# Kernel tuning notes

Hardware: AMD Instinct MI355X
Metric: run time of the kernel (lower is better)

## Reference

```python
import jax, jax.numpy as jnp
from jax import lax
import numpy as np

B, T, I, H = 8192, 365, 3, 34


def setup_inputs() -> dict:
    key = jax.random.key(0)
    ks = jax.random.split(key, 7)
    s_in = 1.0 / np.sqrt(I)
    s_h = 1.0 / np.sqrt(H)
    return {
        "x": jax.random.normal(ks[0], (B, T, I), dtype=jnp.float32),
        "fc0_w": jax.random.uniform(ks[1], (H, I), jnp.float32, -s_in, s_in),
        "fc0_b": jax.random.uniform(ks[2], (H,), jnp.float32, -s_in, s_in),
        "w_ih": jax.random.uniform(ks[3], (4 * H, H), jnp.float32, -s_h, s_h),
        "w_hh": jax.random.uniform(ks[4], (4 * H, H), jnp.float32, -s_h, s_h),
        "b_ih": jax.random.uniform(ks[5], (4 * H,), jnp.float32, -s_h, s_h),
        "b_hh": jax.random.uniform(ks[6], (4 * H,), jnp.float32, -s_h, s_h),
    }


def reference(x, fc0_w, fc0_b, w_ih, w_hh, b_ih, b_hh):
    # fc0: [B,T,I] -> [B,T,H]
    l1 = jnp.einsum("bti,hi->bth", x, fc0_w) + fc0_b
    # Precompute input-side gate projections for all timesteps: [B,T,4H]
    gx = jnp.einsum("bth,gh->btg", l1, w_ih) + b_ih + b_hh
    gx_t = jnp.swapaxes(gx, 0, 1)  # [T,B,4H]

    h0 = jnp.zeros((x.shape[0], fc0_w.shape[0]), dtype=x.dtype)
    c0 = h0

    def step(carry, g_t):
        h, c = carry
        gates = g_t + h @ w_hh.T  # [B,4H]
        i, f, g, o = jnp.split(gates, 4, axis=-1)  # torch gate order: i,f,g,o
        i = jax.nn.sigmoid(i)
        f = jax.nn.sigmoid(f)
        g = jnp.tanh(g)
        o = jax.nn.sigmoid(o)
        c_new = f * c + i * g
        h_new = o * jnp.tanh(c_new)
        return (h_new, c_new), h_new

    (_, _), hs = lax.scan(step, (h0, c0), gx_t)  # hs: [T,B,H]
    return jnp.swapaxes(hs, 0, 1)  # [B,T,H]
```

## Files before the change

kernel.cpp:

```cpp
#include <hip/hip_runtime.h>

namespace {

constexpr int Bn = 8192;
constexpr int Tn = 365;
constexpr int Hn = 34;
constexpr int GB = 16;
constexpr int KP = 72;

constexpr float L2E = 1.44269504088896340736f;

typedef __attribute__((ext_vector_type(8))) _Float16 f16x8;
typedef __attribute__((ext_vector_type(4))) float f32x4;

__device__ __forceinline__ float fexp2(float v) { return __builtin_amdgcn_exp2f(v); }
__device__ __forceinline__ float frcp(float v)  { return __builtin_amdgcn_rcpf(v); }

__device__ __forceinline__ void block_sync_lds() {
    __builtin_amdgcn_sched_barrier(0);
    asm volatile("s_waitcnt lgkmcnt(0)" ::: "memory");
    __builtin_amdgcn_s_barrier();
    __builtin_amdgcn_sched_barrier(0);
}


__global__ __launch_bounds__(256) void lstm_kernel(
    const float* __restrict__ x,
    const float* __restrict__ fc0_w,
    const float* __restrict__ fc0_b,
    const float* __restrict__ w_ih,
    const float* __restrict__ w_hh,
    const float* __restrict__ b_ih,
    const float* __restrict__ b_hh,
    float* __restrict__ out)
{
    __shared__ __align__(16) _Float16 a_lds[2][GB][KP];

    const int tid  = threadIdx.x;
    const int lane = tid & 63;
    const int wv   = tid >> 6;
    const int b    = lane & 15;
    const int kg   = lane >> 4;

    const int nc   = (wv < 2) ? 9 : 8;
    const int base = (wv < 2) ? 9 * wv : 18 + 8 * (wv - 2);

    f16x8 Wt[3][2];
    #pragma unroll
    for (int tau = 0; tau < 3; ++tau) {
        const int rhat = 16 * tau + b;
        const int jl = rhat >> 2, g = rhat & 3;
        const int r = (jl < nc) ? g * Hn + (base + jl) : -1;
        const float s = (g == 2) ? (2.f * L2E) : (-L2E);
        float swc[3] = {0.f, 0.f, 0.f};
        float bia = 0.f;
        if (r >= 0) {
            float ab = 0.f;
            for (int m = 0; m < Hn; ++m) {
                const float wi = w_ih[r * Hn + m];
                swc[0] += wi * fc0_w[m * 3 + 0];
                swc[1] += wi * fc0_w[m * 3 + 1];
                swc[2] += wi * fc0_w[m * 3 + 2];
                ab     += wi * fc0_b[m];
            }
            swc[0] *= s; swc[1] *= s; swc[2] *= s;
            bia = s * (ab + b_ih[r] + b_hh[r]);
        }
        #pragma unroll
        for (int ks = 0; ks < 2; ++ks) {
            f16x8 f;
            #pragma unroll
            for (int e = 0; e < 8; ++e) {
                const int k = ks * 32 + kg * 8 + e;
                float val = 0.f;
                if (r >= 0) {
                    if (k < 34)       val = s * w_hh[r * Hn + k];
                    else if (k < 37)  val = swc[k - 34];
                    else if (k < 40)  val = swc[k - 37];
                    else if (k == 40) val = bia;
                    else if (k == 41) val = bia - (float)(_Float16)bia;
                }
                f[e] = (_Float16)val;
            }
            Wt[tau][ks] = f;
        }
    }

    const bool has2 = (8 + kg < nc);
    float c0 = 0.f, c1 = 0.f, c2 = 0.f;
    float h0 = 0.f, h1 = 0.f, h2 = 0.f;

    const bool xact = (lane < 12);
    const int bx = 4 * wv + lane / 3;
    const int ix = lane - 3 * (lane / 3);

    for (int i = tid; i < 2 * GB * KP; i += 256) ((_Float16*)a_lds)[i] = (_Float16)0.f;
    block_sync_lds();

    const long long bg = (long long)blockIdx.x * GB;
    const float* xblk = x + bg * (long long)(Tn * 3);
    float* oblk = out + bg * (long long)(Tn * Hn);
    const long long TH = (long long)Tn * Hn;

    if (tid < 32) {
        a_lds[tid >> 4][tid & 15][40] = (_Float16)1.f;
        a_lds[tid >> 4][tid & 15][41] = (_Float16)1.f;
    }
    if (xact) {
        const float xr = xblk[bx * (Tn * 3) + ix];
        const _Float16 xh = (_Float16)xr;
        a_lds[0][bx][34 + ix] = xh;
        a_lds[0][bx][37 + ix] = (_Float16)(xr - (float)xh);
    }
    block_sync_lds();

    float xr_hold = 0.f;
    if (xact && 1 < Tn)
        xr_hold = xblk[bx * (Tn * 3) + 3 + ix];

    float* pr = oblk + (long long)b * TH + base;

    for (int t = 0; t < Tn; ++t) {
        const int cur = t & 1, nxt = cur ^ 1;

        f16x8 av[2];
        #pragma unroll
        for (int ks = 0; ks < 2; ++ks)
            av[ks] = *(const f16x8*)(&a_lds[cur][b][ks * 32 + kg * 8]);

        if (xact) {
            const _Float16 xh = (_Float16)xr_hold;
            a_lds[nxt][bx][34 + ix] = xh;
            a_lds[nxt][bx][37 + ix] = (_Float16)(xr_hold - (float)xh);
        }

        if (t) {
            pr[kg]     = h0;
            pr[4 + kg] = h1;
            if (has2) pr[8 + kg] = h2;
            pr += Hn;
        }

        float xr_next = 0.f;
        if (xact && t + 2 < Tn)
            xr_next = xblk[bx * (Tn * 3) + (t + 2) * 3 + ix];

        f32x4 acc[3];
        #pragma unroll
        for (int tau = 0; tau < 3; ++tau) {
            acc[tau] = f32x4{0.f, 0.f, 0.f, 0.f};
            #pragma unroll
            for (int ks = 0; ks < 2; ++ks)
                acc[tau] = __builtin_amdgcn_mfma_f32_16x16x32_f16(Wt[tau][ks], av[ks], acc[tau], 0, 0, 0);
        }

        {
            const float gi = frcp(1.f + fexp2(acc[0][0]));
            const float gf = frcp(1.f + fexp2(acc[0][1]));
            const float gg = fmaf(-2.f, frcp(1.f + fexp2(acc[0][2])), 1.f);
            const float go = frcp(1.f + fexp2(acc[0][3]));
            c0 = gf * c0 + gi * gg;
            h0 = go * fmaf(-2.f, frcp(1.f + fexp2(c0 * (2.f * L2E))), 1.f);
            a_lds[nxt][b][base + kg] = (_Float16)h0;
        }
        {
            const float gi = frcp(1.f + fexp2(acc[1][0]));
            const float gf = frcp(1.f + fexp2(acc[1][1]));
            const float gg = fmaf(-2.f, frcp(1.f + fexp2(acc[1][2])), 1.f);
            const float go = frcp(1.f + fexp2(acc[1][3]));
            c1 = gf * c1 + gi * gg;
            h1 = go * fmaf(-2.f, frcp(1.f + fexp2(c1 * (2.f * L2E))), 1.f);
            a_lds[nxt][b][base + 4 + kg] = (_Float16)h1;
        }
        if (has2) {
            const float gi = frcp(1.f + fexp2(acc[2][0]));
            const float gf = frcp(1.f + fexp2(acc[2][1]));
            const float gg = fmaf(-2.f, frcp(1.f + fexp2(acc[2][2])), 1.f);
            const float go = frcp(1.f + fexp2(acc[2][3]));
            c2 = gf * c2 + gi * gg;
            h2 = go * fmaf(-2.f, frcp(1.f + fexp2(c2 * (2.f * L2E))), 1.f);
            a_lds[nxt][b][base + 8 + kg] = (_Float16)h2;
        }

        xr_hold = xr_next;

        block_sync_lds();
    }

    {
        pr[kg]     = h0;
        pr[4 + kg] = h1;
        if (has2) pr[8 + kg] = h2;
    }
}

}

extern "C" void kernel_launch(void* const* d_in, const int* in_sizes, int n_in,
                              void* d_out, int out_size, void* d_ws, size_t ws_size,
                              hipStream_t stream) {
    const float* x     = (const float*)d_in[0];
    const float* fc0_w = (const float*)d_in[1];
    const float* fc0_b = (const float*)d_in[2];
    const float* w_ih  = (const float*)d_in[3];
    const float* w_hh  = (const float*)d_in[4];
    const float* b_ih  = (const float*)d_in[5];
    const float* b_hh  = (const float*)d_in[6];
    float* out = (float*)d_out;

    lstm_kernel<<<Bn / GB, 256, 0, stream>>>(x, fc0_w, fc0_b, w_ih, w_hh, b_ih, b_hh, out);
}
```

Before: 351.9 us.

## Repartition LSTM cells across 8 waves with 32-batch blocks

Doubles the batch tile per block to 32 and the block size to 512 threads (8 waves). Each wave now owns 4 hidden cells and one gate-weight tile, which it reuses for two batch halves. Wave 7 also handles the last 2 cells. This replaces the old split of 4 waves holding 3 weight tiles each, aiming for fewer wasted MFMA rows and more independent MFMAs per wave. The cost is a heavier load on wave 7 and a block-wide barrier over 8 waves at every timestep.

```diff
diff --git a/kernel.cpp b/kernel.cpp
--- a/kernel.cpp
+++ b/kernel.cpp
@@ -5,7 +5,8 @@
 constexpr int Bn = 8192;
 constexpr int Tn = 365;
 constexpr int Hn = 34;
-constexpr int GB = 16;
+constexpr int GB = 32;
+constexpr int NT = 512;
 constexpr int KP = 72;
 
 constexpr float L2E = 1.44269504088896340736f;
@@ -24,7 +25,7 @@
 }
 
 
-__global__ __launch_bounds__(256) void lstm_kernel(
+__global__ __launch_bounds__(NT) void lstm_kernel(
     const float* __restrict__ x,
     const float* __restrict__ fc0_w,
     const float* __restrict__ fc0_b,
@@ -42,19 +43,19 @@
     const int b    = lane & 15;
     const int kg   = lane >> 4;
 
-    const int nc   = (wv < 2) ? 9 : 8;
-    const int base = (wv < 2) ? 9 * wv : 18 + 8 * (wv - 2);
-
-    f16x8 Wt[3][2];
+    f16x8 Wt[2], Wt2[2];
     #pragma unroll
-    for (int tau = 0; tau < 3; ++tau) {
-        const int rhat = 16 * tau + b;
-        const int jl = rhat >> 2, g = rhat & 3;
-        const int r = (jl < nc) ? g * Hn + (base + jl) : -1;
+    for (int ti = 0; ti < 2; ++ti) {
+        const bool second = (ti == 1);
+        if (second && wv != 7) { Wt2[0] = f16x8{}; Wt2[1] = f16x8{}; continue; }
+        const int cell = second ? (32 + (b >> 2)) : (4 * wv + (b >> 2));
+        const int g    = b & 3;
+        const bool valid = second ? (b < 8) : true;
+        const int r = g * Hn + (valid ? cell : 0);
         const float s = (g == 2) ? (2.f * L2E) : (-L2E);
         float swc[3] = {0.f, 0.f, 0.f};
         float bia = 0.f;
-        if (r >= 0) {
+        if (valid) {
             float ab = 0.f;
             for (int m = 0; m < Hn; ++m) {
                 const float wi = w_ih[r * Hn + m];
@@ -73,7 +74,7 @@
             for (int e = 0; e < 8; ++e) {
                 const int k = ks * 32 + kg * 8 + e;
                 float val = 0.f;
-                if (r >= 0) {
+                if (valid) {
                     if (k < 34)       val = s * w_hh[r * Hn + k];
                     else if (k < 37)  val = swc[k - 34];
                     else if (k < 40)  val = swc[k - 37];
@@ -82,19 +83,22 @@
                 }
                 f[e] = (_Float16)val;
             }
-            Wt[tau][ks] = f;
-        }
-    }
-
-    const bool has2 = (8 + kg < nc);
-    float c0 = 0.f, c1 = 0.f, c2 = 0.f;
-    float h0 = 0.f, h1 = 0.f, h2 = 0.f;
-
-    const bool xact = (lane < 12);
-    const int bx = 4 * wv + lane / 3;
-    const int ix = lane - 3 * (lane / 3);
-
-    for (int i = tid; i < 2 * GB * KP; i += 256) ((_Float16*)a_lds)[i] = (_Float16)0.f;
+            if (second) Wt2[ks] = f; else Wt[ks] = f;
+        }
+    }
+
+    const int j0 = 4 * wv + kg;
+    const bool hasx = (wv == 7) && (kg < 2);
+    const int j1 = 32 + kg;
+
+    float cA0 = 0.f, cB0 = 0.f, hA0 = 0.f, hB0 = 0.f;
+    float cA1 = 0.f, cB1 = 0.f, hA1 = 0.f, hB1 = 0.f;
+
+    const bool xact = (wv < 2) && (lane < 48);
+    const int bxg = wv * 16 + lane / 3;
+    const int ix  = lane - 3 * (lane / 3);
+
+    for (int i = tid; i < 2 * GB * KP; i += NT) ((_Float16*)a_lds)[i] = (_Float16)0.f;
     block_sync_lds();
 
     const long long bg = (long long)blockIdx.x * GB;
@@ -102,84 +106,106 @@
     float* oblk = out + bg * (long long)(Tn * Hn);
     const long long TH = (long long)Tn * Hn;
 
-    if (tid < 32) {
-        a_lds[tid >> 4][tid & 15][40] = (_Float16)1.f;
-        a_lds[tid >> 4][tid & 15][41] = (_Float16)1.f;
-    }
-    if (xact) {
-        const float xr = xblk[bx * (Tn * 3) + ix];
+    if (tid < 64) {
+        a_lds[tid >> 5][tid & 31][40] = (_Float16)1.f;
+        a_lds[tid >> 5][tid & 31][41] = (_Float16)1.f;
+    }
+    if (tid < 96) {
+        const int b32 = tid / 3, i3 = tid - 3 * (tid / 3);
+        const float xr = xblk[b32 * (Tn * 3) + i3];
         const _Float16 xh = (_Float16)xr;
-        a_lds[0][bx][34 + ix] = xh;
-        a_lds[0][bx][37 + ix] = (_Float16)(xr - (float)xh);
+        a_lds[0][b32][34 + i3] = xh;
+        a_lds[0][b32][37 + i3] = (_Float16)(xr - (float)xh);
     }
     block_sync_lds();
 
     float xr_hold = 0.f;
     if (xact && 1 < Tn)
-        xr_hold = xblk[bx * (Tn * 3) + 3 + ix];
-
-    float* pr = oblk + (long long)b * TH + base;
+        xr_hold = xblk[bxg * (Tn * 3) + 3 + ix];
+
+    float* prA = oblk + (long long)b * TH + j0;
+    float* prB = prA + 16 * TH;
+    float* qrA = oblk + (long long)b * TH + j1;
+    float* qrB = qrA + 16 * TH;
 
     for (int t = 0; t < Tn; ++t) {
         const int cur = t & 1, nxt = cur ^ 1;
 
-        f16x8 av[2];
+        f16x8 avA[2], avB[2];
         #pragma unroll
-        for (int ks = 0; ks < 2; ++ks)
-            av[ks] = *(const f16x8*)(&a_lds[cur][b][ks * 32 + kg * 8]);
+        for (int ks = 0; ks < 2; ++ks) {
+            avA[ks] = *(const f16x8*)(&a_lds[cur][b][ks * 32 + kg * 8]);
+            avB[ks] = *(const f16x8*)(&a_lds[cur][16 + b][ks * 32 + kg * 8]);
+        }
 
         if (xact) {
             const _Float16 xh = (_Float16)xr_hold;
-            a_lds[nxt][bx][34 + ix] = xh;
-            a_lds[nxt][bx][37 + ix] = (_Float16)(xr_hold - (float)xh);
+            a_lds[nxt][bxg][34 + ix] = xh;
+            a_lds[nxt][bxg][37 + ix] = (_Float16)(xr_hold - (float)xh);
         }
 
         if (t) {
-            pr[kg]     = h0;
-            pr[4 + kg] = h1;
-            if (has2) pr[8 + kg] = h2;
-            pr += Hn;
+            prA[0] = hA0; prB[0] = hB0;
+            if (hasx) { qrA[0] = hA1; qrB[0] = hB1; }
+            prA += Hn; prB += Hn; qrA += Hn; qrB += Hn;
         }
 
         float xr_next = 0.f;
         if (xact && t + 2 < Tn)
-            xr_next = xblk[bx * (Tn * 3) + (t + 2) * 3 + ix];
-
-        f32x4 acc[3];
+            xr_next = xblk[bxg * (Tn * 3) + (t + 2) * 3 + ix];
+
+        f32x4 aA = {0.f, 0.f, 0.f, 0.f}, aB = {0.f, 0.f, 0.f, 0.f};
         #pragma unroll
-        for (int tau = 0; tau < 3; ++tau) {
-            acc[tau] = f32x4{0.f, 0.f, 0.f, 0.f};
+        for (int ks = 0; ks < 2; ++ks) {
+            aA = __builtin_amdgcn_mfma_f32_16x16x32_f16(Wt[ks], avA[ks], aA, 0, 0, 0);
+            aB = __builtin_amdgcn_mfma_f32_16x16x32_f16(Wt[ks], avB[ks], aB, 0, 0, 0);
+        }
+        f32x4 a2A = {0.f, 0.f, 0.f, 0.f}, a2B = {0.f, 0.f, 0.f, 0.f};
+        if (wv == 7) {
             #pragma unroll
-            for (int ks = 0; ks < 2; ++ks)
-                acc[tau] = __builtin_amdgcn_mfma_f32_16x16x32_f16(Wt[tau][ks], av[ks], acc[tau], 0, 0, 0);
+            for (int ks = 0; ks < 2; ++ks) {
+                a2A = __builtin_amdgcn_mfma_f32_16x16x32_f16(Wt2[ks], avA[ks], a2A, 0, 0, 0);
+                a2B = __builtin_amdgcn_mfma_f32_16x16x32_f16(Wt2[ks], avB[ks], a2B, 0, 0, 0);
+            }
         }
 
         {
-            const float gi = frcp(1.f + fexp2(acc[0][0]));
-            const float gf = frcp(1.f + fexp2(acc[0][1]));
-            const float gg = fmaf(-2.f, frcp(1.f + fexp2(acc[0][2])), 1.f);
-            const float go = frcp(1.f + fexp2(acc[0][3]));
-            c0 = gf * c0 + gi * gg;
-            h0 = go * fmaf(-2.f, frcp(1.f + fexp2(c0 * (2.f * L2E))), 1.f);
-            a_lds[nxt][b][base + kg] = (_Float16)h0;
+            const float gi = frcp(1.f + fexp2(aA[0]));
+            const float gf = frcp(1.f + fexp2(aA[1]));
+            const float gg = fmaf(-2.f, frcp(1.f + fexp2(aA[2])), 1.f);
+            const float go = frcp(1.f + fexp2(aA[3]));
+            cA0 = gf * cA0 + gi * gg;
+            hA0 = go * fmaf(-2.f, frcp(1.f + fexp2(cA0 * (2.f * L2E))), 1.f);
+            a_lds[nxt][b][j0] = (_Float16)hA0;
         }
         {
-            const float gi = frcp(1.f + fexp2(acc[1][0]));
-            const float gf = frcp(1.f + fexp2(acc[1][1]));
-            const float gg = fmaf(-2.f, frcp(1.f + fexp2(acc[1][2])), 1.f);
-            const float go = frcp(1.f + fexp2(acc[1][3]));
-            c1 = gf * c1 + gi * gg;
-            h1 = go * fmaf(-2.f, frcp(1.f + fexp2(c1 * (2.f * L2E))), 1.f);
-            a_lds[nxt][b][base + 4 + kg] = (_Float16)h1;
-        }
-        if (has2) {
-            const float gi = frcp(1.f + fexp2(acc[2][0]));
-            const float gf = frcp(1.f + fexp2(acc[2][1]));
-            const float gg = fmaf(-2.f, frcp(1.f + fexp2(acc[2][2])), 1.f);
-            const float go = frcp(1.f + fexp2(acc[2][3]));
-            c2 = gf * c2 + gi * gg;
-            h2 = go * fmaf(-2.f, frcp(1.f + fexp2(c2 * (2.f * L2E))), 1.f);
-            a_lds[nxt][b][base + 8 + kg] = (_Float16)h2;
+            const float gi = frcp(1.f + fexp2(aB[0]));
+            const float gf = frcp(1.f + fexp2(aB[1]));
+            const float gg = fmaf(-2.f, frcp(1.f + fexp2(aB[2])), 1.f);
+            const float go = frcp(1.f + fexp2(aB[3]));
+            cB0 = gf * cB0 + gi * gg;
+            hB0 = go * fmaf(-2.f, frcp(1.f + fexp2(cB0 * (2.f * L2E))), 1.f);
+            a_lds[nxt][16 + b][j0] = (_Float16)hB0;
+        }
+        if (hasx) {
+            {
+                const float gi = frcp(1.f + fexp2(a2A[0]));
+                const float gf = frcp(1.f + fexp2(a2A[1]));
+                const float gg = fmaf(-2.f, frcp(1.f + fexp2(a2A[2])), 1.f);
+                const float go = frcp(1.f + fexp2(a2A[3]));
+                cA1 = gf * cA1 + gi * gg;
+                hA1 = go * fmaf(-2.f, frcp(1.f + fexp2(cA1 * (2.f * L2E))), 1.f);
+                a_lds[nxt][b][j1] = (_Float16)hA1;
+            }
+            {
+                const float gi = frcp(1.f + fexp2(a2B[0]));
+                const float gf = frcp(1.f + fexp2(a2B[1]));
+                const float gg = fmaf(-2.f, frcp(1.f + fexp2(a2B[2])), 1.f);
+                const float go = frcp(1.f + fexp2(a2B[3]));
+                cB1 = gf * cB1 + gi * gg;
+                hB1 = go * fmaf(-2.f, frcp(1.f + fexp2(cB1 * (2.f * L2E))), 1.f);
+                a_lds[nxt][16 + b][j1] = (_Float16)hB1;
+            }
         }
 
         xr_hold = xr_next;
@@ -188,9 +214,8 @@
     }
 
     {
-        pr[kg]     = h0;
-        pr[4 + kg] = h1;
-        if (has2) pr[8 + kg] = h2;
+        prA[0] = hA0; prB[0] = hB0;
+        if (hasx) { qrA[0] = hA1; qrB[0] = hB1; }
     }
 }
 
@@ -208,5 +233,5 @@
     const float* b_hh  = (const float*)d_in[6];
     float* out = (float*)d_out;
 
-    lstm_kernel<<<Bn / GB, 256, 0, stream>>>(x, fc0_w, fc0_b, w_ih, w_hh, b_ih, b_hh, out);
-}
+    lstm_kernel<<<Bn / GB, NT, 0, stream>>>(x, fc0_w, fc0_b, w_ih, w_hh, b_ih, b_hh, out);
+}
```

New measurement: 374.1 us. 1.06x slower.
